# Optimization experiments

Measured on AMD Instinct MI355X. Metric: run time of the kernel, lower is better.

The kernel has to match this reference:

```python
import jax, jax.numpy as jnp
import numpy as np

K = 3          # deformable kernel size
N = K * K      # sampling points per output pixel
PAD = 1
BN_EPS = 1e-5


def setup_inputs() -> dict:
    key = jax.random.key(0)
    ks = jax.random.split(key, 6)
    B, C, H, W = 32, 103, 32, 32
    Cout = 32
    x = jax.random.normal(ks[0], (B, C, H, W), jnp.float32)
    # offset-predicting conv: 2*N output channels (N y-offsets then N x-offsets)
    w_off = jax.random.normal(ks[1], (2 * N, C, K, K), jnp.float32) * 0.01
    b_off = jnp.zeros((2 * N,), jnp.float32)
    # main deformable conv weight
    w = jax.random.normal(ks[2], (Cout, C, K, K), jnp.float32) * (1.0 / np.sqrt(C * N))
    b = jnp.zeros((Cout,), jnp.float32)
    # BatchNorm (eval mode) params
    gamma = jax.random.uniform(ks[3], (Cout,), jnp.float32, 0.5, 1.5)
    beta = jax.random.normal(ks[4], (Cout,), jnp.float32) * 0.1
    run_mean = jax.random.normal(ks[5], (Cout,), jnp.float32) * 0.1
    run_var = jnp.ones((Cout,), jnp.float32)
    return {"x": x, "w_off": w_off, "b_off": b_off, "w": w, "b": b,
            "gamma": gamma, "beta": beta, "run_mean": run_mean, "run_var": run_var}


def _deform_conv(x, w_off, b_off, w, b):
    B, C, H, W = x.shape
    # predicted offsets: (B, 2N, H, W) -> (B, H, W, N) each for y and x
    off = jax.lax.conv_general_dilated(x, w_off, (1, 1), [(PAD, PAD), (PAD, PAD)])
    off = off + b_off[None, :, None, None]
    off_y = jnp.transpose(off[:, :N], (0, 2, 3, 1))
    off_x = jnp.transpose(off[:, N:], (0, 2, 3, 1))
    # regular kernel grid offsets p_n in {-1,0,1}^2
    ky, kx = jnp.meshgrid(jnp.arange(-1, 2, dtype=jnp.float32),
                          jnp.arange(-1, 2, dtype=jnp.float32), indexing='ij')
    kn_y, kn_x = ky.reshape(-1), kx.reshape(-1)  # (N,)
    # base grid p_0 in padded coordinates (stride 1, padding 1 -> starts at 1)
    p0_y = jnp.arange(1, H + 1, dtype=jnp.float32)[None, :, None, None]
    p0_x = jnp.arange(1, W + 1, dtype=jnp.float32)[None, None, :, None]
    Hp, Wp = H + 2 * PAD, W + 2 * PAD
    py = jnp.clip(p0_y + kn_y + off_y, 0.0, Hp - 1.0)  # (B,H,W,N)
    px = jnp.clip(p0_x + kn_x + off_x, 0.0, Wp - 1.0)
    # zero-padded input, flattened spatial for gather
    xp = jnp.pad(x, ((0, 0), (0, 0), (PAD, PAD), (PAD, PAD)))
    xf = xp.reshape(B, C, Hp * Wp)
    y0 = jnp.clip(jnp.floor(py).astype(jnp.int32), 0, Hp - 2)
    x0 = jnp.clip(jnp.floor(px).astype(jnp.int32), 0, Wp - 2)
    y1, x1 = y0 + 1, x0 + 1
    wy = (py - y0.astype(py.dtype))[:, None]  # (B,1,H,W,N)
    wx = (px - x0.astype(px.dtype))[:, None]

    def gather(yi, xi):
        idx = (yi * Wp + xi).reshape(B, -1)                      # (B, H*W*N)
        g = jnp.take_along_axis(xf, idx[:, None, :], axis=2)    # (B, C, H*W*N)
        return g.reshape(B, C, H, W, N)

    v00, v01 = gather(y0, x0), gather(y0, x1)
    v10, v11 = gather(y1, x0), gather(y1, x1)
    samp = (v00 * (1 - wy) * (1 - wx) + v01 * (1 - wy) * wx
            + v10 * wy * (1 - wx) + v11 * wy * wx)               # (B,C,H,W,N)
    out = jnp.einsum('bchwn,ocn->bohw', samp, w.reshape(w.shape[0], C, N))
    return out + b[None, :, None, None]


def reference(x, w_off, b_off, w, b, gamma, beta, run_mean, run_var):
    out = _deform_conv(x, w_off, b_off, w, b)
    # BatchNorm2d (eval mode) + ReLU
    inv = gamma * jax.lax.rsqrt(run_var + BN_EPS)
    out = out * inv[None, :, None, None] + (beta - run_mean * inv)[None, :, None, None]
    return jax.nn.relu(out)
```

## Files before the change

kernel.cpp:

```cpp
#include <hip/hip_runtime.h>


#define CC    103
#define COUT  32
#define KSC   5
#define RSU   34
#define GS_D  4656
#define BUF_U (2 * GS_D)

typedef __attribute__((ext_vector_type(8))) _Float16 f16x8;
typedef __attribute__((ext_vector_type(2))) _Float16 h2;
typedef __attribute__((ext_vector_type(2))) __fp16  fp16x2;
typedef __attribute__((ext_vector_type(4))) float f32x4;
typedef __attribute__((ext_vector_type(4))) unsigned int u32x4;

#define WTPM_W 0
#define WTPO_W 17920
#define BN_W   35840
#define XPK_W  35904

__global__ void k_prep(const float* __restrict__ x,
                       const float* __restrict__ w, const float* __restrict__ w_off,
                       const float* __restrict__ bias, const float* __restrict__ gamma,
                       const float* __restrict__ beta, const float* __restrict__ mean,
                       const float* __restrict__ var,
                       unsigned short* __restrict__ wtpm, unsigned short* __restrict__ wtpo,
                       float* __restrict__ bn, unsigned int* __restrict__ xpk) {
    int bx = blockIdx.x;
    if (bx < 280) {
        int tid = bx * 256 + threadIdx.x;
        if (tid < 71680) {
            int half_ = tid >= 35840 ? 1 : 0;
            int e = tid - half_ * 35840;
            const float* src = half_ ? w_off : w;
            unsigned short* dst = half_ ? wtpo : wtpm;
            int mrows = half_ ? 18 : 32;
            int j = e & 7, lane = (e >> 3) & 63, tile = e >> 9;
            int mt = tile & 1, chs = tile >> 1;
            int s = chs % 5, ch = chs / 5;
            int o = mt * 16 + (lane & 15);
            int kl = s * 32 + (lane >> 4) * 8 + j;
            int n = kl >> 4, c = ch * 16 + (kl & 15);
            float v = 0.f;
            if (n < 9 && c < CC && o < mrows) v = src[o * (CC * 9) + c * 9 + n];
            union { _Float16 h; unsigned short u; } cv;
            cv.h = (_Float16)v;
            dst[e] = cv.u;
        }
        if (tid < 32) {
            float inv = gamma[tid] * rsqrtf(var[tid] + 1e-5f);
            bn[tid]      = inv;
            bn[32 + tid] = beta[tid] + (bias[tid] - mean[tid]) * inv;
        }
    } else {
        int pb = bx - 280;
        int b = pb / 7, ch = pb - b * 7;
        int tl = threadIdx.x;
        const float* xb = x + b * (CC * 1024) + tl * 4;
        unsigned int* dst = xpk + pb * 8192 + tl * 16;
        unsigned d[8][4];
#pragma unroll
        for (int i = 0; i < 8; i++) {
            int c = ch * 16 + 2 * i;
            float4 L = make_float4(0.f, 0.f, 0.f, 0.f);
            float4 M = make_float4(0.f, 0.f, 0.f, 0.f);
            if (c < CC)     L = *(const float4*)(xb + c * 1024);
            if (c + 1 < CC) M = *(const float4*)(xb + (c + 1) * 1024);
            union { fp16x2 hh; unsigned u; } p0, p1, p2, p3;
            p0.hh = __builtin_amdgcn_cvt_pkrtz(L.x, M.x);
            p1.hh = __builtin_amdgcn_cvt_pkrtz(L.y, M.y);
            p2.hh = __builtin_amdgcn_cvt_pkrtz(L.z, M.z);
            p3.hh = __builtin_amdgcn_cvt_pkrtz(L.w, M.w);
            d[i][0] = p0.u; d[i][1] = p1.u; d[i][2] = p2.u; d[i][3] = p3.u;
        }
#pragma unroll
        for (int q = 0; q < 4; q++) {
            *(u32x4*)(dst + q * 4)        = (u32x4){d[0][q], d[1][q], d[2][q], d[3][q]};
            *(u32x4*)(dst + 4096 + q * 4) = (u32x4){d[4][q], d[5][q], d[6][q], d[7][q]};
        }
    }
}

__global__ void __launch_bounds__(512, 4)
k_fused(const unsigned int* __restrict__ xpk, const float* __restrict__ b_off,
        const unsigned short* __restrict__ wtpo, const unsigned short* __restrict__ wtpm,
        const float* __restrict__ bn, float* __restrict__ out) {
    __shared__ __align__(16) unsigned int ldsp[2 * BUF_U];
    __shared__ float exch[18 * 64];

    int bid = blockIdx.x;
    int b   = (bid & 7) * 4 + ((bid >> 3) & 3);
    int pxg = bid >> 5;

    int t = threadIdx.x, lane = t & 63, wv = t >> 6;
    int kh = wv >> 2;
    int pxl = (wv & 3) * 16 + (lane & 15);
    int px  = pxg * 64 + pxl;
    int h = px >> 5, wq = px & 31;
    int kg = lane >> 4;
    int hi = kg >> 1;
    int kgrp = kg & 1;

    unsigned int* mybuf = ldsp + kh * BUF_U;

    int tl = t & 255;
    int r = tl >> 3, c = tl & 7;

    int r0 = 2 * pxg - 1; if (r0 < 0) r0 = 0;
    int r1 = 2 * pxg + 2; if (r1 > 31) r1 = 31;
    bool rowact = (r >= r0 && r <= r1);

    const int KYL[5] = {0,0,1,2,2}, KXL[5] = {0,2,1,0,2};
    const int KYH[5] = {0,1,1,2,2}, KXH[5] = {1,0,2,1,2};
    const int TAPL[5] = {0,2,4,6,8}, TAPH[5] = {1,3,5,7,8};
    int myky[5], mykx[5], mytap[5];
#pragma unroll
    for (int s = 0; s < 5; s++) {
        myky[s] = hi ? KYH[s] : KYL[s];
        mykx[s] = hi ? KXH[s] : KXL[s];
        mytap[s] = hi ? TAPH[s] : TAPL[s];
    }

    u32x4 U[8];
    auto loadx = [&](int ch, bool full) {
        if (!full && !rowact) return;
        const unsigned int* s0 = xpk + (b * 7 + ch) * 8192 + (r * 32 + c) * 4;
#pragma unroll
        for (int g = 0; g < 2; g++)
#pragma unroll
        for (int k = 0; k < 4; k++)
            U[g * 4 + k] = __builtin_nontemporal_load(
                               (const u32x4*)(s0 + g * 4096 + k * 32));
    };
    auto packwrite = [&](int ch, bool full) {
        if (!full && !rowact) return;
        unsigned int* dstb = mybuf + ((r + 1) * RSU + 2 + c) * 4;
#pragma unroll
        for (int g = 0; g < 2; g++)
#pragma unroll
        for (int k = 0; k < 4; k++)
            *(u32x4*)(dstb + g * GS_D + k * 32) = U[g * 4 + k];
    };

    auto chunk1 = [&](int it) { return kh ? (2 * it) : (it < 3 ? 2 * it + 1 : -1); };
    auto chunk2 = [&](int it) { return kh ? (6 - 2 * it) : (it < 3 ? 5 - 2 * it : -1); };
    int fullIt = 2 + kh;

    f32x4 acc0 = {0.f, 0.f, 0.f, 0.f};
    f32x4 acc1 = {0.f, 0.f, 0.f, 0.f};

    loadx(chunk1(0), false);
    {
        u32x4 z4 = (u32x4){0u, 0u, 0u, 0u};
        for (int i = t; i < 560; i += 512) {
            int grp = i / 140, rr = i - grp * 140;
            int off;
            if (rr < 34)      off = rr;
            else if (rr < 76) off = 1122 + (rr - 34);
            else { int q2 = (rr - 76) >> 1; off = (q2 + 1) * 34 + ((rr - 76) & 1); }
            *(u32x4*)(ldsp + (grp >> 1) * BUF_U + (grp & 1) * GS_D + off * 4) = z4;
        }
    }
    __syncthreads();

    for (int it = 0; it < 4; it++) {
        int ch = chunk1(it);
        if (ch >= 0) packwrite(ch, it == fullIt);
        __syncthreads();
        int nx = (it < 3) ? chunk1(it + 1) : -1;
        if (nx >= 0) loadx(nx, it + 1 == fullIt);
        if (ch >= 0) {
            const unsigned short* wch = wtpo + ch * 5120;
#pragma unroll
            for (int s = 0; s < KSC; s++) {
                const unsigned int* cell = mybuf + kgrp * GS_D
                    + ((h + myky[s]) * RSU + 1 + (wq + mykx[s])) * 4;
                union { u32x4 q; f16x8 v; } bu;
                bu.q = *(const u32x4*)cell;
                f16x8 a0 = *(const f16x8*)(wch + s * 1024 + lane * 8);
                f16x8 a1 = *(const f16x8*)(wch + s * 1024 + 512 + lane * 8);
                acc0 = __builtin_amdgcn_mfma_f32_16x16x32_f16(a0, bu.v, acc0, 0, 0, 0);
                acc1 = __builtin_amdgcn_mfma_f32_16x16x32_f16(a1, bu.v, acc1, 0, 0, 0);
            }
        }
        __syncthreads();
    }

    if (kh == 0) {
        float* ex = exch + pxl;
#pragma unroll
        for (int reg = 0; reg < 4; reg++) ex[(kg * 4 + reg) * 64] = acc0[reg];
        if (kg == 0) { ex[16 * 64] = acc1[0]; ex[17 * 64] = acc1[1]; }
    }
    __syncthreads();
    if (kh == 1) {
        float* ex = exch + pxl;
#pragma unroll
        for (int reg = 0; reg < 4; reg++) ex[(kg * 4 + reg) * 64] += acc0[reg];
        if (kg == 0) { ex[16 * 64] += acc1[0]; ex[17 * 64] += acc1[1]; }
    }
    __syncthreads();

    int cofs[KSC];
    h2  W[KSC][4];
#pragma unroll
    for (int s = 0; s < KSC; s++) {
        int tap = mytap[s];
        float oy = exch[tap * 64 + pxl] + b_off[tap];
        float ox = exch[(9 + tap) * 64 + pxl] + b_off[9 + tap];
        float py  = (float)(h + myky[s]) + oy;
        float pxx = (float)(wq + mykx[s]) + ox;
        py  = fminf(fmaxf(py, 0.f), 33.f);
        pxx = fminf(fmaxf(pxx, 0.f), 33.f);
        int y0 = min((int)py, 32);
        int x0 = min((int)pxx, 32);
        float fy = py - (float)y0;
        float fx = pxx - (float)x0;
        float w00 = (1.f - fy) * (1.f - fx), w01 = (1.f - fy) * fx;
        float w10 = fy * (1.f - fx),          w11 = fy * fx;
        W[s][0] = (h2){(_Float16)w00, (_Float16)w00};
        W[s][1] = (h2){(_Float16)w01, (_Float16)w01};
        W[s][2] = (h2){(_Float16)w10, (_Float16)w10};
        W[s][3] = (h2){(_Float16)w11, (_Float16)w11};
        cofs[s] = kgrp * GS_D + (y0 * RSU + 1 + x0) * 4;
    }

    acc0 = (f32x4){0.f, 0.f, 0.f, 0.f};
    acc1 = (f32x4){0.f, 0.f, 0.f, 0.f};
    for (int it = 0; it < 4; it++) {
        int ch = chunk2(it);
        if (it > 0) {
            if (ch >= 0) packwrite(ch, true);
            else {
                float* e = (float*)ldsp + pxl;
#pragma unroll
                for (int reg = 0; reg < 4; reg++) {
                    e[(kg * 4 + reg) * 64]      = acc0[reg];
                    e[(16 + kg * 4 + reg) * 64] = acc1[reg];
                }
            }
        }
        __syncthreads();
        int nx = (it < 3) ? chunk2(it + 1) : -1;
        if (nx >= 0) loadx(nx, true);
        if (ch >= 0) {
            const unsigned short* wch = wtpm + ch * 5120;
#pragma unroll
            for (int s = 0; s < KSC; s++) {
                const unsigned int* cell = mybuf + cofs[s];
                union { u32x4 q; unsigned a[4]; } T0, T1, B0, B1;
                T0.q = *(const u32x4*)(cell);
                T1.q = *(const u32x4*)(cell + 4);
                B0.q = *(const u32x4*)(cell + 4 * RSU);
                B1.q = *(const u32x4*)(cell + 4 * RSU + 4);
                union { unsigned u[4]; f16x8 v; } bu;
#pragma unroll
                for (int jj = 0; jj < 4; jj++) {
                    union { unsigned u; h2 hh; } t0, t1, b0, b1, rr;
                    t0.u = T0.a[jj];
                    t1.u = T1.a[jj];
                    b0.u = B0.a[jj];
                    b1.u = B1.a[jj];
                    rr.hh = t0.hh * W[s][0] + t1.hh * W[s][1]
                          + b0.hh * W[s][2] + b1.hh * W[s][3];
                    bu.u[jj] = rr.u;
                }
                f16x8 a0 = *(const f16x8*)(wch + s * 1024 + lane * 8);
                f16x8 a1 = *(const f16x8*)(wch + s * 1024 + 512 + lane * 8);
                acc0 = __builtin_amdgcn_mfma_f32_16x16x32_f16(a0, bu.v, acc0, 0, 0, 0);
                acc1 = __builtin_amdgcn_mfma_f32_16x16x32_f16(a1, bu.v, acc1, 0, 0, 0);
            }
        }
        __syncthreads();
    }

    if (kh == 1) {
        const float* ex2 = (const float*)ldsp;
        float* op = out + (size_t)b * COUT * 1024 + px;
#pragma unroll
        for (int mt = 0; mt < 2; mt++) {
            f32x4 a = mt ? acc1 : acc0;
#pragma unroll
            for (int reg = 0; reg < 4; reg++) {
                int o = mt * 16 + kg * 4 + reg;
                float tot = a[reg] + ex2[o * 64 + pxl];
                float v = tot * bn[o] + bn[32 + o];
                __builtin_nontemporal_store(fmaxf(v, 0.f), &op[o * 1024]);
            }
        }
    }
}

extern "C" void kernel_launch(void* const* d_in, const int* in_sizes, int n_in,
                              void* d_out, int out_size, void* d_ws, size_t ws_size,
                              hipStream_t stream) {
    const float* x      = (const float*)d_in[0];
    const float* w_off  = (const float*)d_in[1];
    const float* b_off  = (const float*)d_in[2];
    const float* w      = (const float*)d_in[3];
    const float* bias   = (const float*)d_in[4];
    const float* gamma  = (const float*)d_in[5];
    const float* beta   = (const float*)d_in[6];
    const float* rmean  = (const float*)d_in[7];
    const float* rvar   = (const float*)d_in[8];
    float* out = (float*)d_out;

    float* ws = (float*)d_ws;
    unsigned short* wtpm = (unsigned short*)(ws + WTPM_W);
    unsigned short* wtpo = (unsigned short*)(ws + WTPO_W);
    float*          bn   = ws + BN_W;
    unsigned int*   xpk  = (unsigned int*)(ws + XPK_W);

    k_prep <<<504, 256, 0, stream>>>(x, w, w_off, bias, gamma, beta, rmean, rvar,
                                     wtpm, wtpo, bn, xpk);
    k_fused<<<512, 512, 0, stream>>>(xpk, b_off, wtpo, wtpm, bn, out);
}
```

Measured before the change: 102.0 us.

## Store packed input in padded LDS layout and read offset-conv taps from global

The prep kernel now writes the fp16-packed input directly in the padded, halo-zeroed tile layout used in shared memory. The offset-conv phase then loads its 5 tap cells per chunk straight from global memory, double-buffered in registers, and no longer stages chunks through LDS with a barrier per iteration. The stage-2 loads copy the padded layout verbatim. This removes LDS staging and barriers from the first phase, at the cost of more global and cache traffic and a larger packed buffer.

```diff
diff --git a/kernel.cpp b/kernel.cpp
--- a/kernel.cpp
+++ b/kernel.cpp
@@ -57,7 +57,7 @@
         int b = pb / 7, ch = pb - b * 7;
         int tl = threadIdx.x;
         const float* xb = x + b * (CC * 1024) + tl * 4;
-        unsigned int* dst = xpk + pb * 8192 + tl * 16;
+        unsigned int* dstp = xpk + pb * BUF_U;
         unsigned d[8][4];
 #pragma unroll
         for (int i = 0; i < 8; i++) {
@@ -73,10 +73,21 @@
             p3.hh = __builtin_amdgcn_cvt_pkrtz(L.w, M.w);
             d[i][0] = p0.u; d[i][1] = p1.u; d[i][2] = p2.u; d[i][3] = p3.u;
         }
+        int row = tl >> 3, col = (tl & 7) * 4;
+        int slot0 = (row + 1) * 34 + 2 + col;
 #pragma unroll
         for (int q = 0; q < 4; q++) {
-            *(u32x4*)(dst + q * 4)        = (u32x4){d[0][q], d[1][q], d[2][q], d[3][q]};
-            *(u32x4*)(dst + 4096 + q * 4) = (u32x4){d[4][q], d[5][q], d[6][q], d[7][q]};
+            *(u32x4*)(dstp + (slot0 + q) * 4)        = (u32x4){d[0][q], d[1][q], d[2][q], d[3][q]};
+            *(u32x4*)(dstp + GS_D + (slot0 + q) * 4) = (u32x4){d[4][q], d[5][q], d[6][q], d[7][q]};
+        }
+        u32x4 z4 = (u32x4){0u, 0u, 0u, 0u};
+        for (int i = tl; i < 280; i += 256) {
+            int g = i / 140, rr = i - g * 140;
+            int slot;
+            if (rr < 34)      slot = rr;
+            else if (rr < 76) slot = 1122 + (rr - 34);
+            else { int k2 = (rr - 76) >> 1; slot = (k2 + 1) * 34 + ((rr - 76) & 1); }
+            *(u32x4*)(dstp + g * GS_D + slot * 4) = z4;
         }
     }
 }
@@ -102,38 +113,34 @@
     int kgrp = kg & 1;
 
     unsigned int* mybuf = ldsp + kh * BUF_U;
+    const unsigned int* xpb = xpk + b * 7 * BUF_U;
 
     int tl = t & 255;
     int r = tl >> 3, c = tl & 7;
-
-    int r0 = 2 * pxg - 1; if (r0 < 0) r0 = 0;
-    int r1 = 2 * pxg + 2; if (r1 > 31) r1 = 31;
-    bool rowact = (r >= r0 && r <= r1);
 
     const int KYL[5] = {0,0,1,2,2}, KXL[5] = {0,2,1,0,2};
     const int KYH[5] = {0,1,1,2,2}, KXH[5] = {1,0,2,1,2};
     const int TAPL[5] = {0,2,4,6,8}, TAPH[5] = {1,3,5,7,8};
-    int myky[5], mykx[5], mytap[5];
+    int myky[5], mykx[5], mytap[5], rel1[5];
 #pragma unroll
     for (int s = 0; s < 5; s++) {
         myky[s] = hi ? KYH[s] : KYL[s];
         mykx[s] = hi ? KXH[s] : KXL[s];
         mytap[s] = hi ? TAPH[s] : TAPL[s];
+        rel1[s] = kgrp * GS_D + ((h + myky[s]) * RSU + 1 + (wq + mykx[s])) * 4;
     }
 
     u32x4 U[8];
-    auto loadx = [&](int ch, bool full) {
-        if (!full && !rowact) return;
-        const unsigned int* s0 = xpk + (b * 7 + ch) * 8192 + (r * 32 + c) * 4;
+    auto loadx = [&](int ch) {
+        const unsigned int* s0 = xpb + ch * BUF_U + ((r + 1) * RSU + 2 + c) * 4;
 #pragma unroll
         for (int g = 0; g < 2; g++)
 #pragma unroll
         for (int k = 0; k < 4; k++)
             U[g * 4 + k] = __builtin_nontemporal_load(
-                               (const u32x4*)(s0 + g * 4096 + k * 32));
+                               (const u32x4*)(s0 + g * GS_D + k * 32));
     };
-    auto packwrite = [&](int ch, bool full) {
-        if (!full && !rowact) return;
+    auto packwrite = [&]() {
         unsigned int* dstb = mybuf + ((r + 1) * RSU + 2 + c) * 4;
 #pragma unroll
         for (int g = 0; g < 2; g++)
@@ -144,12 +151,12 @@
 
     auto chunk1 = [&](int it) { return kh ? (2 * it) : (it < 3 ? 2 * it + 1 : -1); };
     auto chunk2 = [&](int it) { return kh ? (6 - 2 * it) : (it < 3 ? 5 - 2 * it : -1); };
-    int fullIt = 2 + kh;
 
     f32x4 acc0 = {0.f, 0.f, 0.f, 0.f};
     f32x4 acc1 = {0.f, 0.f, 0.f, 0.f};
 
-    loadx(chunk1(0), false);
+    loadx(chunk2(0));
+
     {
         u32x4 z4 = (u32x4){0u, 0u, 0u, 0u};
         for (int i = t; i < 560; i += 512) {
@@ -161,29 +168,37 @@
             *(u32x4*)(ldsp + (grp >> 1) * BUF_U + (grp & 1) * GS_D + off * 4) = z4;
         }
     }
-    __syncthreads();
-
-    for (int it = 0; it < 4; it++) {
-        int ch = chunk1(it);
-        if (ch >= 0) packwrite(ch, it == fullIt);
-        __syncthreads();
-        int nx = (it < 3) ? chunk1(it + 1) : -1;
-        if (nx >= 0) loadx(nx, it + 1 == fullIt);
-        if (ch >= 0) {
-            const unsigned short* wch = wtpo + ch * 5120;
-#pragma unroll
-            for (int s = 0; s < KSC; s++) {
-                const unsigned int* cell = mybuf + kgrp * GS_D
-                    + ((h + myky[s]) * RSU + 1 + (wq + mykx[s])) * 4;
-                union { u32x4 q; f16x8 v; } bu;
-                bu.q = *(const u32x4*)cell;
-                f16x8 a0 = *(const f16x8*)(wch + s * 1024 + lane * 8);
-                f16x8 a1 = *(const f16x8*)(wch + s * 1024 + 512 + lane * 8);
-                acc0 = __builtin_amdgcn_mfma_f32_16x16x32_f16(a0, bu.v, acc0, 0, 0, 0);
-                acc1 = __builtin_amdgcn_mfma_f32_16x16x32_f16(a1, bu.v, acc1, 0, 0, 0);
+
+    {
+        u32x4 P0[KSC], P1[KSC];
+        auto issue5 = [&](int ch, u32x4* P) {
+            const unsigned int* s0 = xpb + ch * BUF_U;
+#pragma unroll
+            for (int s = 0; s < KSC; s++)
+                P[s] = __builtin_nontemporal_load((const u32x4*)(s0 + rel1[s]));
+        };
+        issue5(chunk1(0), P0);
+        packwrite();
+#pragma unroll
+        for (int it = 0; it < 4; it++) {
+            int ch = chunk1(it);
+            int nx = (it < 3) ? chunk1(it + 1) : -1;
+            u32x4* P = (it & 1) ? P1 : P0;
+            u32x4* Q = (it & 1) ? P0 : P1;
+            if (nx >= 0) issue5(nx, Q);
+            if (ch >= 0) {
+                const unsigned short* wch = wtpo + ch * 5120;
+#pragma unroll
+                for (int s = 0; s < KSC; s++) {
+                    union { u32x4 q; f16x8 v; } bu;
+                    bu.q = P[s];
+                    f16x8 a0 = *(const f16x8*)(wch + s * 1024 + lane * 8);
+                    f16x8 a1 = *(const f16x8*)(wch + s * 1024 + 512 + lane * 8);
+                    acc0 = __builtin_amdgcn_mfma_f32_16x16x32_f16(a0, bu.v, acc0, 0, 0, 0);
+                    acc1 = __builtin_amdgcn_mfma_f32_16x16x32_f16(a1, bu.v, acc1, 0, 0, 0);
+                }
             }
         }
-        __syncthreads();
     }
 
     if (kh == 0) {
@@ -230,7 +245,7 @@
     for (int it = 0; it < 4; it++) {
         int ch = chunk2(it);
         if (it > 0) {
-            if (ch >= 0) packwrite(ch, true);
+            if (ch >= 0) packwrite();
             else {
                 float* e = (float*)ldsp + pxl;
 #pragma unroll
@@ -242,7 +257,7 @@
         }
         __syncthreads();
         int nx = (it < 3) ? chunk2(it + 1) : -1;
-        if (nx >= 0) loadx(nx, true);
+        if (nx >= 0) loadx(nx);
         if (ch >= 0) {
             const unsigned short* wch = wtpm + ch * 5120;
 #pragma unroll
```

Result: slower. 104.8 us (+2.8%).
